# Optimization experiments

Measured on AMD Instinct MI355X. Metric: run time of the kernel, lower is better.

## Reference

```python
import jax, jax.numpy as jnp
import numpy as np

E = 300000        # num_edges
T = 3000000       # num_triplets
D = 128           # edge_message_dim
N_RAD = 6
N_SPH = 7
D_DOWN = 64       # edge_down_dim
D_BAS = 8         # basis_embed_dim


def _w(key, fan_in, fan_out):
    return jax.random.normal(key, (fan_in, fan_out), jnp.float32) / np.sqrt(fan_in)


def setup_inputs() -> dict:
    key = jax.random.key(0)
    ks = jax.random.split(key, 32)
    inp = {
        "x": jax.random.normal(ks[0], (E, D), jnp.float32),
        "rbf": jax.random.uniform(ks[1], (E, N_RAD), jnp.float32),
        "sbf": jax.random.uniform(ks[2], (T, N_SPH * N_RAD), jnp.float32),
        "idx_kj": jax.random.randint(ks[3], (T,), 0, E),
        "idx_ji": jax.random.randint(ks[4], (T,), 0, E),
        # basis projections (bias-free)
        "w_rbf1": _w(ks[5], N_RAD, D_BAS),
        "w_rbf2": _w(ks[6], D_BAS, D),
        "w_sbf1": _w(ks[7], N_SPH * N_RAD, D_BAS),
        "w_sbf2": _w(ks[8], D_BAS, D_DOWN),
        # message linears (with bias)
        "w_kj": _w(ks[9], D, D), "b_kj": jnp.zeros((D,), jnp.float32),
        "w_ji": _w(ks[10], D, D), "b_ji": jnp.zeros((D,), jnp.float32),
        # down / up projections (bias-free)
        "w_down": _w(ks[11], D, D_DOWN),
        "w_up": _w(ks[12], D_DOWN, D),
        # residual block before skip + dense
        "res1_w1": _w(ks[13], D, D), "res1_b1": jnp.zeros((D,), jnp.float32),
        "res1_w2": _w(ks[14], D, D), "res1_b2": jnp.zeros((D,), jnp.float32),
        "w_bs": _w(ks[15], D, D), "b_bs": jnp.zeros((D,), jnp.float32),
        # two residual blocks after skip
        "res2_w1": _w(ks[16], D, D), "res2_b1": jnp.zeros((D,), jnp.float32),
        "res2_w2": _w(ks[17], D, D), "res2_b2": jnp.zeros((D,), jnp.float32),
        "res3_w1": _w(ks[18], D, D), "res3_b1": jnp.zeros((D,), jnp.float32),
        "res3_w2": _w(ks[19], D, D), "res3_b2": jnp.zeros((D,), jnp.float32),
    }
    return inp


def _res_block(h, w1, b1, w2, b2):
    # h + act(lin2(act(lin1(h)))) with Swish(beta=1) == silu
    return h + jax.nn.silu(jax.nn.silu(h @ w1 + b1) @ w2 + b2)


def reference(x, rbf, sbf, idx_kj, idx_ji,
              w_rbf1, w_rbf2, w_sbf1, w_sbf2,
              w_kj, b_kj, w_ji, b_ji, w_down, w_up,
              res1_w1, res1_b1, res1_w2, res1_b2, w_bs, b_bs,
              res2_w1, res2_b1, res2_w2, res2_b2,
              res3_w1, res3_b1, res3_w2, res3_b2):
    act = jax.nn.silu
    x_ji = act(x @ w_ji + b_ji)                       # [E, D]
    x_kj = act(x @ w_kj + b_kj)                       # [E, D]
    rbf_e = (rbf @ w_rbf1) @ w_rbf2                   # [E, D]
    x_kj = act((x_kj * rbf_e) @ w_down)               # [E, D_DOWN]
    sbf_e = (sbf @ w_sbf1) @ w_sbf2                   # [T, D_DOWN]
    m = x_kj[idx_kj] * sbf_e                          # gather + Hadamard [T, D_DOWN]
    agg = jax.ops.segment_sum(m, idx_ji, num_segments=x.shape[0])  # [E, D_DOWN]
    x_kj = act(agg @ w_up)                            # [E, D]
    h = _res_block(x_ji + x_kj, res1_w1, res1_b1, res1_w2, res1_b2)
    h = act(h @ w_bs + b_bs) + x                      # skip connection
    h = _res_block(h, res2_w1, res2_b1, res2_w2, res2_b2)
    h = _res_block(h, res3_w1, res3_b1, res3_w2, res3_b2)
    return h
```

## Files before the change

kernel.cpp:

```cpp
#include <hip/hip_runtime.h>
#include <hip/hip_bf16.h>


typedef __attribute__((ext_vector_type(8))) short bf16x8;
typedef __attribute__((ext_vector_type(4))) float f32x4;
typedef __attribute__((ext_vector_type(4))) unsigned int u32x4;

__device__ __forceinline__ float silu_f(float v) {
    return v * __builtin_amdgcn_rcpf(1.0f + __expf(-v));
}
__device__ __forceinline__ short f2bf(float f) {
    unsigned u = __float_as_uint(f);
    unsigned r = u + 0x7fffu + ((u >> 16) & 1u);
    return (short)(r >> 16);
}
__device__ __forceinline__ float bf2f(short s) {
    return __uint_as_float(((unsigned)(unsigned short)s) << 16);
}

__device__ __forceinline__ unsigned cvt_pk_bf16(float a, float b) {
    __hip_bfloat162 h = __float22bfloat162_rn(float2{a, b});
    return *reinterpret_cast<unsigned*>(&h);
}
__device__ __forceinline__ void split44(f32x4 a, f32x4 b, bf16x8& hi, bf16x8& lo) {
    float f[8] = {a[0], a[1], a[2], a[3], b[0], b[1], b[2], b[3]};
    u32x4 H, L;
    #pragma unroll
    for (int j = 0; j < 4; ++j) {
        const float f0 = f[2 * j], f1 = f[2 * j + 1];
        const unsigned h = cvt_pk_bf16(f0, f1);
        const float r0 = f0 - __uint_as_float(h << 16);
        const float r1 = f1 - __uint_as_float(h & 0xffff0000u);
        H[j] = h;
        L[j] = cvt_pk_bf16(r0, r1);
    }
    hi = __builtin_bit_cast(bf16x8, H);
    lo = __builtin_bit_cast(bf16x8, L);
}

__device__ __forceinline__ void gll16(const void* g, void* l) {
    __builtin_amdgcn_global_load_lds((const __attribute__((address_space(1))) void*)g,
                                     (__attribute__((address_space(3))) void*)l, 16, 0, 0);
}
__device__ __forceinline__ void stage16(const char* g, short* l, int lane, int wid) {
    #pragma unroll
    for (int i = 0; i < 4; ++i) {
        const int off = ((i * 4 + wid) << 10);
        gll16(g + off + lane * 16, (char*)l + off);
    }
}
__device__ __forceinline__ void stage8(const char* g, short* l, int lane, int wid) {
    #pragma unroll
    for (int i = 0; i < 2; ++i) {
        const int off = ((i * 4 + wid) << 10);
        gll16(g + off + lane * 16, (char*)l + off);
    }
}

template<int NF>
__device__ __forceinline__ void mfma_ks(bf16x8 ah, bf16x8 al, const short* slot,
                                        int acol, int kq, f32x4* acc) {
    #pragma unroll
    for (int n = 0; n < NF; ++n) {
        const int c = n * 16 + acol;
        const int x = (c >> 2) & 1;
        const int sw = (kq ^ (c & 3)) << 3;
        const bf16x8 bh = *(const bf16x8*)&slot[c * 64 + x * 32 + sw];
        const bf16x8 bl = *(const bf16x8*)&slot[c * 64 + (x ^ 1) * 32 + sw];
        acc[n] = __builtin_amdgcn_mfma_f32_16x16x32_bf16(ah, bh, acc[n], 0, 0, 0);
        acc[n] = __builtin_amdgcn_mfma_f32_16x16x32_bf16(al, bh, acc[n], 0, 0, 0);
        acc[n] = __builtin_amdgcn_mfma_f32_16x16x32_bf16(ah, bl, acc[n], 0, 0, 0);
    }
}

__device__ __forceinline__ void tfrag(const float* tl, int rb, int q, int kq,
                                      bf16x8& Ah, bf16x8& Al) {
    const f32x4 ta = *(const f32x4*)&tl[rb + q * 32 + kq * 8];
    const f32x4 tb = *(const f32x4*)&tl[rb + q * 32 + kq * 8 + 4];
    split44(ta, tb, Ah, Al);
}

__device__ __forceinline__ void tgemm4(const char* img, const char* imgnext,
                                       short* sA, short* sB, const float* tl, int rb,
                                       int kq, int acol, int lane, int wid, f32x4* acc)
{
    bf16x8 Ah[4], Al[4];
    #pragma unroll
    for (int q = 0; q < 4; ++q) tfrag(tl, rb, q, kq, Ah[q], Al[q]);

    stage16(img + 16384, sB, lane, wid);
    mfma_ks<8>(Ah[0], Al[0], sA, acol, kq, acc); __syncthreads();
    stage16(img + 32768, sA, lane, wid);
    mfma_ks<8>(Ah[1], Al[1], sB, acol, kq, acc); __syncthreads();
    stage16(img + 49152, sB, lane, wid);
    mfma_ks<8>(Ah[2], Al[2], sA, acol, kq, acc); __syncthreads();
    if (imgnext) stage16(imgnext, sA, lane, wid);
    mfma_ks<8>(Ah[3], Al[3], sB, acol, kq, acc); __syncthreads();
}

#define TPITCH 132

struct WDesc { const float* src; char* dst; int K; int N; };
struct WPrepArgs { WDesc w[11]; };

__global__ void wprep_kernel(WPrepArgs args) {
    const WDesc d = args.w[blockIdx.y];
    const int h = blockIdx.x;
    if (h * 32 >= d.K) return;
    char* slab = d.dst + (size_t)h * d.N * 128;
    for (int idx = threadIdx.x; idx < d.N * 4; idx += 256) {
        const int c = idx >> 2, ch = idx & 3;
        bf16x8 hi, lo;
        #pragma unroll
        for (int j = 0; j < 8; ++j) {
            const float f = d.src[(size_t)(h * 32 + ch * 8 + j) * d.N + c];
            const short hb = f2bf(f);
            hi[j] = hb;
            lo[j] = f2bf(f - bf2f(hb));
        }
        const int x = (c >> 2) & 1;
        const int sw = (ch ^ (c & 3)) * 16;
        *(bf16x8*)(slab + c * 128 + x * 64 + sw)       = hi;
        *(bf16x8*)(slab + c * 128 + (x ^ 1) * 64 + sw) = lo;
    }
}


__global__ void rbf1_kernel(const float* __restrict__ rbf, const float* __restrict__ w_rbf1,
                            float* __restrict__ re1, int E) {
    const int i = blockIdx.x * 256 + threadIdx.x;
    const int e = i >> 3, p = i & 7;
    if (e < E) {
        float s = 0.f;
        #pragma unroll
        for (int q = 0; q < 6; ++q) s = fmaf(rbf[e * 6 + q], w_rbf1[q * 8 + p], s);
        re1[i] = s;
    }
}

__global__ void count_rank_kernel(const int* __restrict__ idx_ji, int* __restrict__ cnt,
                                  int* __restrict__ rank, int T) {
    const int i = (blockIdx.x * 256 + threadIdx.x) * 4;
    if (i + 3 < T) {
        const int4 j = *(const int4*)&idx_ji[i];
        int4 r;
        r.x = atomicAdd(&cnt[j.x], 1);
        r.y = atomicAdd(&cnt[j.y], 1);
        r.z = atomicAdd(&cnt[j.z], 1);
        r.w = atomicAdd(&cnt[j.w], 1);
        *(int4*)&rank[i] = r;
    } else {
        for (int k = i; k < T; ++k) rank[k] = atomicAdd(&cnt[idx_ji[k]], 1);
    }
}

__global__ void scan_partial_kernel(const int* __restrict__ cnt, int* __restrict__ partial, int E) {
    __shared__ int red[256];
    const int tid = threadIdx.x;
    const int base = blockIdx.x * 1024 + tid * 4;
    int s = 0;
    #pragma unroll
    for (int i = 0; i < 4; ++i) { const int g = base + i; if (g < E) s += cnt[g]; }
    red[tid] = s;
    __syncthreads();
    for (int off = 128; off > 0; off >>= 1) {
        if (tid < off) red[tid] += red[tid + off];
        __syncthreads();
    }
    if (tid == 0) partial[blockIdx.x] = red[0];
}

__global__ void scan_block_kernel(const int* __restrict__ partial, int* __restrict__ blockoff,
                                  int NB, int* offsets, int E) {
    __shared__ int red[256];
    const int tid = threadIdx.x;
    int v[4]; int s = 0;
    #pragma unroll
    for (int i = 0; i < 4; ++i) { const int g = tid * 4 + i; v[i] = (g < NB) ? partial[g] : 0; s += v[i]; }
    red[tid] = s;
    __syncthreads();
    for (int off = 1; off < 256; off <<= 1) {
        const int add = (tid >= off) ? red[tid - off] : 0;
        __syncthreads();
        red[tid] += add;
        __syncthreads();
    }
    int excl = (tid == 0) ? 0 : red[tid - 1];
    #pragma unroll
    for (int i = 0; i < 4; ++i) { const int g = tid * 4 + i; if (g < NB) blockoff[g] = excl; excl += v[i]; }
    if (tid == 255) offsets[E] = red[255];
}

__global__ void scan_final_kernel(const int* __restrict__ cnt, const int* __restrict__ blockoff,
                                  int* __restrict__ offsets, int E) {
    __shared__ int red[256];
    const int tid = threadIdx.x;
    const int base = blockIdx.x * 1024 + tid * 4;
    int v[4]; int s = 0;
    #pragma unroll
    for (int i = 0; i < 4; ++i) { const int g = base + i; v[i] = (g < E) ? cnt[g] : 0; s += v[i]; }
    red[tid] = s;
    __syncthreads();
    for (int off = 1; off < 256; off <<= 1) {
        const int add = (tid >= off) ? red[tid - off] : 0;
        __syncthreads();
        red[tid] += add;
        __syncthreads();
    }
    int run = blockoff[blockIdx.x] + ((tid == 0) ? 0 : red[tid - 1]);
    #pragma unroll
    for (int i = 0; i < 4; ++i) {
        const int g = base + i;
        if (g < E) offsets[g] = run;
        run += v[i];
    }
}

__launch_bounds__(256, 3)
__global__ void e1fill_kernel(const float* __restrict__ sbf, const float* __restrict__ w_sbf1,
                              const int* __restrict__ idx_ji, const int* __restrict__ idx_kj,
                              const int* __restrict__ rank, const int* __restrict__ offsets,
                              float* __restrict__ E1p, int* __restrict__ kjp, int T)
{
    __shared__ float s_lds[256 * 43];
    const int tid = threadIdx.x;
    const long long t0 = (long long)blockIdx.x * 256;
    const int nrow = min(256, (int)(T - t0));
    const int nel  = nrow * 42;
    const float* base = sbf + t0 * 42;

    for (int i = tid * 4; i + 3 < nel; i += 1024) {
        const float4 v = *(const float4*)&base[i];
        s_lds[(i + 0) + (i + 0) / 42] = v.x;
        s_lds[(i + 1) + (i + 1) / 42] = v.y;
        s_lds[(i + 2) + (i + 2) / 42] = v.z;
        s_lds[(i + 3) + (i + 3) / 42] = v.w;
    }
    const int tail0 = nel & ~3;
    if (tid < nel - tail0) { const int g = tail0 + tid; s_lds[g + g / 42] = base[g]; }
    __syncthreads();

    const int t = (int)t0 + tid;
    if (t >= T) return;
    const float* srow = &s_lds[tid * 43];
    float e1[8] = {0.f, 0.f, 0.f, 0.f, 0.f, 0.f, 0.f, 0.f};
    #pragma unroll
    for (int q = 0; q < 42; ++q) {
        const float s = srow[q];
        #pragma unroll
        for (int p = 0; p < 8; ++p) e1[p] = fmaf(s, w_sbf1[q * 8 + p], e1[p]);
    }
    const int ji  = idx_ji[t];
    const int pos = offsets[ji] + rank[t];
    *(float4*)&E1p[(size_t)pos * 8]     = *(float4*)&e1[0];
    *(float4*)&E1p[(size_t)pos * 8 + 4] = *(float4*)&e1[4];
    kjp[pos] = idx_kj[t];
}

__launch_bounds__(256, 4)
__global__ void gather_kernel(const float* __restrict__ E1p, const int* __restrict__ kjp,
                              const float* __restrict__ w_sbf2, const int* __restrict__ offsets,
                              const float* __restrict__ xkjd, float* __restrict__ agg, int E)
{
    const int tid  = threadIdx.x;
    const int lane = tid & 63;
    const int e    = blockIdx.x * 4 + (tid >> 6);

    float w2[8];
    #pragma unroll
    for (int p = 0; p < 8; ++p) w2[p] = w_sbf2[p * 64 + lane];

    if (e >= E) return;
    const int j0 = __builtin_amdgcn_readfirstlane(offsets[e]);
    const int j1 = __builtin_amdgcn_readfirstlane(offsets[e + 1]);

    float acc = 0.f;
    if (j0 < j1) {
        int kj = __builtin_amdgcn_readfirstlane(kjp[j0]);
        float4 ea = *(const float4*)&E1p[(size_t)j0 * 8];
        float4 eb = *(const float4*)&E1p[(size_t)j0 * 8 + 4];
        float xv = xkjd[(size_t)kj * 64 + lane];
        for (int j = j0; j < j1; ++j) {
            float xn = 0.f; float4 ean = {}, ebn = {};
            if (j + 1 < j1) {
                const int kn = __builtin_amdgcn_readfirstlane(kjp[j + 1]);
                ean = *(const float4*)&E1p[(size_t)(j + 1) * 8];
                ebn = *(const float4*)&E1p[(size_t)(j + 1) * 8 + 4];
                xn  = xkjd[(size_t)kn * 64 + lane];
            }
            float sv = ea.x * w2[0];
            sv = fmaf(ea.y, w2[1], sv);
            sv = fmaf(ea.z, w2[2], sv);
            sv = fmaf(ea.w, w2[3], sv);
            sv = fmaf(eb.x, w2[4], sv);
            sv = fmaf(eb.y, w2[5], sv);
            sv = fmaf(eb.z, w2[6], sv);
            sv = fmaf(eb.w, w2[7], sv);
            acc = fmaf(xv, sv, acc);
            ea = ean; eb = ebn; xv = xn;
        }
    }
    agg[(size_t)e * 64 + lane] = acc;
}

__launch_bounds__(256, 2)
__global__ void k1_kernel(const float* __restrict__ x, const char* __restrict__ wkj_i,
                          const float* __restrict__ b_kj, const float* __restrict__ re1,
                          const float* __restrict__ w_rbf2, const char* __restrict__ wdn_i,
                          float* __restrict__ W3, int E)
{
    __shared__ short slotA[8192], slotB[8192];
    __shared__ float t_lds[64 * TPITCH];
    __shared__ float w2_lds[8 * 128];
    const int tid = threadIdx.x, lane = tid & 63, wid = tid >> 6;
    const int acol = lane & 15, kq = lane >> 4;
    const int rowW = blockIdx.x * 64 + wid * 16;
    const int arow = rowW + acol;
    const bool av = arow < E;

    stage16(wkj_i, slotA, lane, wid);
    const float* xr = x + (size_t)arow * 128;
    bf16x8 aH[4], aL[4];
    #pragma unroll
    for (int ks = 0; ks < 4; ++ks) {
        f32x4 a0 = f32x4{0.f, 0.f, 0.f, 0.f}, a1 = f32x4{0.f, 0.f, 0.f, 0.f};
        if (av) { a0 = *(const f32x4*)&xr[ks * 32 + kq * 8];
                  a1 = *(const f32x4*)&xr[ks * 32 + kq * 8 + 4]; }
        split44(a0, a1, aH[ks], aL[ks]);
    }
    float bv[8];
    #pragma unroll
    for (int n = 0; n < 8; ++n) bv[n] = b_kj[n * 16 + acol];
    f32x4 e1a[4], e1b[4];
    #pragma unroll
    for (int r = 0; r < 4; ++r) {
        const int ge = rowW + kq * 4 + r;
        e1a[r] = f32x4{0.f, 0.f, 0.f, 0.f}; e1b[r] = f32x4{0.f, 0.f, 0.f, 0.f};
        if (ge < E) { e1a[r] = *(const f32x4*)&re1[(size_t)ge * 8];
                      e1b[r] = *(const f32x4*)&re1[(size_t)ge * 8 + 4]; }
    }
    for (int i = tid; i < 1024; i += 256) w2_lds[i] = w_rbf2[i];
    __syncthreads();

    f32x4 acc[8];
    #pragma unroll
    for (int n = 0; n < 8; ++n) acc[n] = f32x4{0.f, 0.f, 0.f, 0.f};

    stage16(wkj_i + 16384, slotB, lane, wid);
    mfma_ks<8>(aH[0], aL[0], slotA, acol, kq, acc); __syncthreads();
    stage16(wkj_i + 32768, slotA, lane, wid);
    mfma_ks<8>(aH[1], aL[1], slotB, acol, kq, acc); __syncthreads();
    stage16(wkj_i + 49152, slotB, lane, wid);
    mfma_ks<8>(aH[2], aL[2], slotA, acol, kq, acc); __syncthreads();
    stage8(wdn_i, slotA, lane, wid);
    mfma_ks<8>(aH[3], aL[3], slotB, acol, kq, acc); __syncthreads();

    #pragma unroll
    for (int n = 0; n < 8; ++n) {
        const int c = n * 16 + acol;
        float w2c[8];
        #pragma unroll
        for (int p = 0; p < 8; ++p) w2c[p] = w2_lds[p * 128 + c];
        #pragma unroll
        for (int r = 0; r < 4; ++r) {
            float s = e1a[r][0] * w2c[0];
            s = fmaf(e1a[r][1], w2c[1], s);
            s = fmaf(e1a[r][2], w2c[2], s);
            s = fmaf(e1a[r][3], w2c[3], s);
            s = fmaf(e1b[r][0], w2c[4], s);
            s = fmaf(e1b[r][1], w2c[5], s);
            s = fmaf(e1b[r][2], w2c[6], s);
            s = fmaf(e1b[r][3], w2c[7], s);
            t_lds[(wid * 16 + kq * 4 + r) * TPITCH + c] = silu_f(acc[n][r] + bv[n]) * s;
        }
    }
    __syncthreads();

    f32x4 acc2[4];
    #pragma unroll
    for (int n = 0; n < 4; ++n) acc2[n] = f32x4{0.f, 0.f, 0.f, 0.f};
    const int rb = (wid * 16 + acol) * TPITCH;

    bf16x8 tH[4], tL[4];
    #pragma unroll
    for (int q = 0; q < 4; ++q) tfrag(t_lds, rb, q, kq, tH[q], tL[q]);

    stage8(wdn_i + 8192, slotB, lane, wid);
    mfma_ks<4>(tH[0], tL[0], slotA, acol, kq, acc2); __syncthreads();
    stage8(wdn_i + 16384, slotA, lane, wid);
    mfma_ks<4>(tH[1], tL[1], slotB, acol, kq, acc2); __syncthreads();
    stage8(wdn_i + 24576, slotB, lane, wid);
    mfma_ks<4>(tH[2], tL[2], slotA, acol, kq, acc2); __syncthreads();
    mfma_ks<4>(tH[3], tL[3], slotB, acol, kq, acc2);

    #pragma unroll
    for (int n = 0; n < 4; ++n) {
        const int c = n * 16 + acol;
        #pragma unroll
        for (int r = 0; r < 4; ++r) {
            const int ge = rowW + kq * 4 + r;
            if (ge < E) W3[(size_t)ge * 64 + c] = silu_f(acc2[n][r]);
        }
    }
}

struct KBigArgs {
    const float* x; const float* W4; float* out;
    const char *wji, *wup, *r1w1, *r1w2, *wbs, *r2w1, *r2w2, *r3w1, *r3w2;
    const float *bji, *r1b1, *r1b2, *bbs, *r2b1, *r2b2, *r3b1, *r3b2;
    int E;
};

__launch_bounds__(256, 2)
__global__ void kbig_kernel(KBigArgs A_)
{
    __shared__ short slotA[8192], slotB[8192];
    __shared__ float t_lds[64 * TPITCH];
    const int tid = threadIdx.x, lane = tid & 63, wid = tid >> 6;
    const int acol = lane & 15, kq = lane >> 4;
    const int rowW = blockIdx.x * 64 + wid * 16;
    const int arow = rowW + acol;
    const int E = A_.E;
    const bool av = arow < E;
    const int rb = (wid * 16 + acol) * TPITCH;

    stage16(A_.wji, slotA, lane, wid);

    const float* xr = A_.x + (size_t)arow * 128;
    const float* wr = A_.W4 + (size_t)arow * 64;
    bf16x8 aH[4], aL[4], uH[2], uL[2];
    #pragma unroll
    for (int ks = 0; ks < 4; ++ks) {
        f32x4 a0 = f32x4{0.f, 0.f, 0.f, 0.f}, a1 = f32x4{0.f, 0.f, 0.f, 0.f};
        if (av) { a0 = *(const f32x4*)&xr[ks * 32 + kq * 8];
                  a1 = *(const f32x4*)&xr[ks * 32 + kq * 8 + 4]; }
        split44(a0, a1, aH[ks], aL[ks]);
    }
    #pragma unroll
    for (int ks = 0; ks < 2; ++ks) {
        f32x4 u0 = f32x4{0.f, 0.f, 0.f, 0.f}, u1 = f32x4{0.f, 0.f, 0.f, 0.f};
        if (av) { u0 = *(const f32x4*)&wr[ks * 32 + kq * 8];
                  u1 = *(const f32x4*)&wr[ks * 32 + kq * 8 + 4]; }
        split44(u0, u1, uH[ks], uL[ks]);
    }
    __syncthreads();

    f32x4 acc[8];
    #pragma unroll
    for (int n = 0; n < 8; ++n) acc[n] = f32x4{0.f, 0.f, 0.f, 0.f};

    stage16(A_.wji + 16384, slotB, lane, wid);
    mfma_ks<8>(aH[0], aL[0], slotA, acol, kq, acc); __syncthreads();
    stage16(A_.wji + 32768, slotA, lane, wid);
    mfma_ks<8>(aH[1], aL[1], slotB, acol, kq, acc); __syncthreads();
    stage16(A_.wji + 49152, slotB, lane, wid);
    mfma_ks<8>(aH[2], aL[2], slotA, acol, kq, acc); __syncthreads();
    stage16(A_.wup, slotA, lane, wid);
    mfma_ks<8>(aH[3], aL[3], slotB, acol, kq, acc); __syncthreads();

    float res[8][4];
    #pragma unroll
    for (int n = 0; n < 8; ++n) {
        const float bv = A_.bji[n * 16 + acol];
        #pragma unroll
        for (int r = 0; r < 4; ++r) { res[n][r] = silu_f(acc[n][r] + bv); acc[n][r] = 0.f; }
    }

    stage16(A_.wup + 16384, slotB, lane, wid);
    mfma_ks<8>(uH[0], uL[0], slotA, acol, kq, acc); __syncthreads();
    stage16(A_.r1w1, slotA, lane, wid);
    mfma_ks<8>(uH[1], uL[1], slotB, acol, kq, acc); __syncthreads();

    #pragma unroll
    for (int n = 0; n < 8; ++n) {
        const int c = n * 16 + acol;
        #pragma unroll
        for (int r = 0; r < 4; ++r) {
            res[n][r] += silu_f(acc[n][r]);
            t_lds[(wid * 16 + kq * 4 + r) * TPITCH + c] = res[n][r];
            acc[n][r] = 0.f;
        }
    }
    __syncthreads();

    tgemm4(A_.r1w1, A_.r1w2, slotA, slotB, t_lds, rb, kq, acol, lane, wid, acc);
    #pragma unroll
    for (int n = 0; n < 8; ++n) {
        const float bv = A_.r1b1[n * 16 + acol];
        const int c = n * 16 + acol;
        #pragma unroll
        for (int r = 0; r < 4; ++r) {
            t_lds[(wid * 16 + kq * 4 + r) * TPITCH + c] = silu_f(acc[n][r] + bv);
            acc[n][r] = 0.f;
        }
    }
    __syncthreads();

    tgemm4(A_.r1w2, A_.wbs, slotA, slotB, t_lds, rb, kq, acol, lane, wid, acc);
    #pragma unroll
    for (int n = 0; n < 8; ++n) {
        const float bv = A_.r1b2[n * 16 + acol];
        const int c = n * 16 + acol;
        #pragma unroll
        for (int r = 0; r < 4; ++r) {
            t_lds[(wid * 16 + kq * 4 + r) * TPITCH + c] = res[n][r] + silu_f(acc[n][r] + bv);
            acc[n][r] = 0.f;
        }
    }
    __syncthreads();

    tgemm4(A_.wbs, A_.r2w1, slotA, slotB, t_lds, rb, kq, acol, lane, wid, acc);
    #pragma unroll
    for (int n = 0; n < 8; ++n) {
        const float bv = A_.bbs[n * 16 + acol];
        const int c = n * 16 + acol;
        #pragma unroll
        for (int r = 0; r < 4; ++r) {
            const int ge = rowW + kq * 4 + r;
            const float xv = (ge < E) ? A_.x[(size_t)ge * 128 + c] : 0.f;
            res[n][r] = silu_f(acc[n][r] + bv) + xv;
            t_lds[(wid * 16 + kq * 4 + r) * TPITCH + c] = res[n][r];
            acc[n][r] = 0.f;
        }
    }
    __syncthreads();

    tgemm4(A_.r2w1, A_.r2w2, slotA, slotB, t_lds, rb, kq, acol, lane, wid, acc);
    #pragma unroll
    for (int n = 0; n < 8; ++n) {
        const float bv = A_.r2b1[n * 16 + acol];
        const int c = n * 16 + acol;
        #pragma unroll
        for (int r = 0; r < 4; ++r) {
            t_lds[(wid * 16 + kq * 4 + r) * TPITCH + c] = silu_f(acc[n][r] + bv);
            acc[n][r] = 0.f;
        }
    }
    __syncthreads();

    tgemm4(A_.r2w2, A_.r3w1, slotA, slotB, t_lds, rb, kq, acol, lane, wid, acc);
    #pragma unroll
    for (int n = 0; n < 8; ++n) {
        const float bv = A_.r2b2[n * 16 + acol];
        const int c = n * 16 + acol;
        #pragma unroll
        for (int r = 0; r < 4; ++r) {
            res[n][r] += silu_f(acc[n][r] + bv);
            t_lds[(wid * 16 + kq * 4 + r) * TPITCH + c] = res[n][r];
            acc[n][r] = 0.f;
        }
    }
    __syncthreads();

    tgemm4(A_.r3w1, A_.r3w2, slotA, slotB, t_lds, rb, kq, acol, lane, wid, acc);
    #pragma unroll
    for (int n = 0; n < 8; ++n) {
        const float bv = A_.r3b1[n * 16 + acol];
        const int c = n * 16 + acol;
        #pragma unroll
        for (int r = 0; r < 4; ++r) {
            t_lds[(wid * 16 + kq * 4 + r) * TPITCH + c] = silu_f(acc[n][r] + bv);
            acc[n][r] = 0.f;
        }
    }
    __syncthreads();

    tgemm4(A_.r3w2, nullptr, slotA, slotB, t_lds, rb, kq, acol, lane, wid, acc);
    #pragma unroll
    for (int n = 0; n < 8; ++n) {
        const float bv = A_.r3b2[n * 16 + acol];
        const int c = n * 16 + acol;
        #pragma unroll
        for (int r = 0; r < 4; ++r) {
            const int ge = rowW + kq * 4 + r;
            if (ge < E)
                A_.out[(size_t)ge * 128 + c] = res[n][r] + silu_f(acc[n][r] + bv);
        }
    }
}


extern "C" void kernel_launch(void* const* d_in, const int* in_sizes, int n_in,
                              void* d_out, int out_size, void* d_ws, size_t ws_size,
                              hipStream_t stream)
{
    const float* x      = (const float*)d_in[0];
    const float* rbf    = (const float*)d_in[1];
    const float* sbf    = (const float*)d_in[2];
    const int*   idx_kj = (const int*)d_in[3];
    const int*   idx_ji = (const int*)d_in[4];
    const float* w_rbf1 = (const float*)d_in[5];
    const float* w_rbf2 = (const float*)d_in[6];
    const float* w_sbf1 = (const float*)d_in[7];
    const float* w_sbf2 = (const float*)d_in[8];
    const float* w_kj   = (const float*)d_in[9];
    const float* b_kj   = (const float*)d_in[10];
    const float* w_ji   = (const float*)d_in[11];
    const float* b_ji   = (const float*)d_in[12];
    const float* w_down = (const float*)d_in[13];
    const float* w_up   = (const float*)d_in[14];
    const float* r1w1   = (const float*)d_in[15];
    const float* r1b1   = (const float*)d_in[16];
    const float* r1w2   = (const float*)d_in[17];
    const float* r1b2   = (const float*)d_in[18];
    const float* w_bs   = (const float*)d_in[19];
    const float* b_bs   = (const float*)d_in[20];
    const float* r2w1   = (const float*)d_in[21];
    const float* r2b1   = (const float*)d_in[22];
    const float* r2w2   = (const float*)d_in[23];
    const float* r2b2   = (const float*)d_in[24];
    const float* r3w1   = (const float*)d_in[25];
    const float* r3b1   = (const float*)d_in[26];
    const float* r3w2   = (const float*)d_in[27];
    const float* r3b2   = (const float*)d_in[28];

    const int E = in_sizes[0] / 128;
    const int T = in_sizes[2] / 42;

    float* OUT = (float*)d_out;
    float* W3  = (float*)((char*)d_ws + (size_t)E * 128 * 4);
    float* W4  = (float*)((char*)d_ws + (size_t)E * 128 * 4
                                      + (size_t)E * 64 * 4);

    int*   cnt      = (int*)d_ws;
    int*   offsets  = cnt + (E + 64);
    int*   partial  = offsets + (E + 64);
    int*   blockoff = partial + 1024;
    float* E1p      = (float*)((char*)d_ws + (4u << 20));
    int*   kjp      = (int*)((char*)d_ws + (102u << 20));
    float* re1      = (float*)((char*)d_ws + (116u << 20));
    char*  wimg     = (char*)d_ws + (130u << 20);
    int*   rank     = (int*)((char*)d_ws + (134u << 20));

    char* wkj_i  = wimg;
    char* wji_i  = wimg + 65536;
    char* wdn_i  = wimg + 131072;
    char* wup_i  = wimg + 163840;
    char* r1w1_i = wimg + 196608;
    char* r1w2_i = wimg + 262144;
    char* wbs_i  = wimg + 327680;
    char* r2w1_i = wimg + 393216;
    char* r2w2_i = wimg + 458752;
    char* r3w1_i = wimg + 524288;
    char* r3w2_i = wimg + 589824;

    WPrepArgs pa;
    pa.w[0]  = {w_kj,   wkj_i,  128, 128};
    pa.w[1]  = {w_ji,   wji_i,  128, 128};
    pa.w[2]  = {w_down, wdn_i,  128,  64};
    pa.w[3]  = {w_up,   wup_i,   64, 128};
    pa.w[4]  = {r1w1,   r1w1_i, 128, 128};
    pa.w[5]  = {r1w2,   r1w2_i, 128, 128};
    pa.w[6]  = {w_bs,   wbs_i,  128, 128};
    pa.w[7]  = {r2w1,   r2w1_i, 128, 128};
    pa.w[8]  = {r2w2,   r2w2_i, 128, 128};
    pa.w[9]  = {r3w1,   r3w1_i, 128, 128};
    pa.w[10] = {r3w2,   r3w2_i, 128, 128};

    const dim3 b256(256);
    const int gB  = (E + 63) / 64;
    const int gT  = (T + 255) / 256;
    const int gT4 = (T + 1023) / 1024;
    const int NB  = (E + 1023) / 1024;
    const int gE4 = (E + 3) / 4;
    const int gR  = (E * 8 + 255) / 256;

    wprep_kernel<<<dim3(4, 11), b256, 0, stream>>>(pa);
    rbf1_kernel<<<gR, b256, 0, stream>>>(rbf, w_rbf1, re1, E);
    hipMemsetAsync(cnt, 0, (size_t)E * 4, stream);
    count_rank_kernel<<<gT4, b256, 0, stream>>>(idx_ji, cnt, rank, T);
    scan_partial_kernel<<<NB, b256, 0, stream>>>(cnt, partial, E);
    scan_block_kernel<<<1, b256, 0, stream>>>(partial, blockoff, NB, offsets, E);
    scan_final_kernel<<<NB, b256, 0, stream>>>(cnt, blockoff, offsets, E);
    e1fill_kernel<<<gT, b256, 0, stream>>>(sbf, w_sbf1, idx_ji, idx_kj, rank, offsets, E1p, kjp, T);

    k1_kernel<<<gB, b256, 0, stream>>>(x, wkj_i, b_kj, re1, w_rbf2, wdn_i, W3, E);
    gather_kernel<<<gE4, b256, 0, stream>>>(E1p, kjp, w_sbf2, offsets, W3, W4, E);

    KBigArgs ka;
    ka.x = x; ka.W4 = W4; ka.out = OUT;
    ka.wji = wji_i; ka.wup = wup_i; ka.r1w1 = r1w1_i; ka.r1w2 = r1w2_i; ka.wbs = wbs_i;
    ka.r2w1 = r2w1_i; ka.r2w2 = r2w2_i; ka.r3w1 = r3w1_i; ka.r3w2 = r3w2_i;
    ka.bji = b_ji; ka.r1b1 = r1b1; ka.r1b2 = r1b2; ka.bbs = b_bs;
    ka.r2b1 = r2b1; ka.r2b2 = r2b2; ka.r3b1 = r3b1; ka.r3b2 = r3b2;
    ka.E = E;
    kbig_kernel<<<gB, b256, 0, stream>>>(ka);
}
```

Baseline: 1.201 ms.

## Switch dense GEMMs from 3-pass bf16 split to 2-pass fp16 split

Replaces the bf16 hi/lo split (three MFMAs per tile: hi*hi, lo*hi, hi*lo) with an fp16 scheme: activations are split into fp16 hi/lo, weights are stored as a single fp16 copy, and two MFMAs run per tile. This halves the weight image size and the LDS staging buffers, and drops a third of the MFMA work. The smaller LDS footprint allows raising launch bounds to 3 blocks per CU for higher occupancy. The risk is reduced accuracy: weights carry only fp16 precision, and fp16's narrower exponent range could overflow or underflow on large or tiny activations.

```diff
diff --git a/kernel.cpp b/kernel.cpp
--- a/kernel.cpp
+++ b/kernel.cpp
@@ -2,99 +2,74 @@
 #include <hip/hip_bf16.h>
 
 
-typedef __attribute__((ext_vector_type(8))) short bf16x8;
+typedef __attribute__((ext_vector_type(8))) _Float16 f16x8;
 typedef __attribute__((ext_vector_type(4))) float f32x4;
-typedef __attribute__((ext_vector_type(4))) unsigned int u32x4;
 
 __device__ __forceinline__ float silu_f(float v) {
     return v * __builtin_amdgcn_rcpf(1.0f + __expf(-v));
 }
-__device__ __forceinline__ short f2bf(float f) {
-    unsigned u = __float_as_uint(f);
-    unsigned r = u + 0x7fffu + ((u >> 16) & 1u);
-    return (short)(r >> 16);
-}
-__device__ __forceinline__ float bf2f(short s) {
-    return __uint_as_float(((unsigned)(unsigned short)s) << 16);
-}
-
-__device__ __forceinline__ unsigned cvt_pk_bf16(float a, float b) {
-    __hip_bfloat162 h = __float22bfloat162_rn(float2{a, b});
-    return *reinterpret_cast<unsigned*>(&h);
-}
-__device__ __forceinline__ void split44(f32x4 a, f32x4 b, bf16x8& hi, bf16x8& lo) {
+
+__device__ __forceinline__ void split44h(f32x4 a, f32x4 b, f16x8& hi, f16x8& lo) {
     float f[8] = {a[0], a[1], a[2], a[3], b[0], b[1], b[2], b[3]};
-    u32x4 H, L;
-    #pragma unroll
-    for (int j = 0; j < 4; ++j) {
-        const float f0 = f[2 * j], f1 = f[2 * j + 1];
-        const unsigned h = cvt_pk_bf16(f0, f1);
-        const float r0 = f0 - __uint_as_float(h << 16);
-        const float r1 = f1 - __uint_as_float(h & 0xffff0000u);
-        H[j] = h;
-        L[j] = cvt_pk_bf16(r0, r1);
-    }
-    hi = __builtin_bit_cast(bf16x8, H);
-    lo = __builtin_bit_cast(bf16x8, L);
+    #pragma unroll
+    for (int j = 0; j < 8; ++j) {
+        const _Float16 h = (_Float16)f[j];
+        hi[j] = h;
+        lo[j] = (_Float16)(f[j] - (float)h);
+    }
 }
 
 __device__ __forceinline__ void gll16(const void* g, void* l) {
     __builtin_amdgcn_global_load_lds((const __attribute__((address_space(1))) void*)g,
                                      (__attribute__((address_space(3))) void*)l, 16, 0, 0);
 }
-__device__ __forceinline__ void stage16(const char* g, short* l, int lane, int wid) {
-    #pragma unroll
-    for (int i = 0; i < 4; ++i) {
-        const int off = ((i * 4 + wid) << 10);
-        gll16(g + off + lane * 16, (char*)l + off);
-    }
-}
-__device__ __forceinline__ void stage8(const char* g, short* l, int lane, int wid) {
+__device__ __forceinline__ void stage8k(const char* g, _Float16* l, int lane, int wid) {
     #pragma unroll
     for (int i = 0; i < 2; ++i) {
         const int off = ((i * 4 + wid) << 10);
         gll16(g + off + lane * 16, (char*)l + off);
     }
 }
+__device__ __forceinline__ void stage4k(const char* g, _Float16* l, int lane, int wid) {
+    const int off = (wid << 10);
+    gll16(g + off + lane * 16, (char*)l + off);
+}
 
 template<int NF>
-__device__ __forceinline__ void mfma_ks(bf16x8 ah, bf16x8 al, const short* slot,
+__device__ __forceinline__ void mfma_ks(f16x8 ah, f16x8 al, const _Float16* slot,
                                         int acol, int kq, f32x4* acc) {
     #pragma unroll
     for (int n = 0; n < NF; ++n) {
         const int c = n * 16 + acol;
-        const int x = (c >> 2) & 1;
         const int sw = (kq ^ (c & 3)) << 3;
-        const bf16x8 bh = *(const bf16x8*)&slot[c * 64 + x * 32 + sw];
-        const bf16x8 bl = *(const bf16x8*)&slot[c * 64 + (x ^ 1) * 32 + sw];
-        acc[n] = __builtin_amdgcn_mfma_f32_16x16x32_bf16(ah, bh, acc[n], 0, 0, 0);
-        acc[n] = __builtin_amdgcn_mfma_f32_16x16x32_bf16(al, bh, acc[n], 0, 0, 0);
-        acc[n] = __builtin_amdgcn_mfma_f32_16x16x32_bf16(ah, bl, acc[n], 0, 0, 0);
+        const f16x8 bh = *(const f16x8*)&slot[c * 32 + sw];
+        acc[n] = __builtin_amdgcn_mfma_f32_16x16x32_f16(ah, bh, acc[n], 0, 0, 0);
+        acc[n] = __builtin_amdgcn_mfma_f32_16x16x32_f16(al, bh, acc[n], 0, 0, 0);
     }
 }
 
 __device__ __forceinline__ void tfrag(const float* tl, int rb, int q, int kq,
-                                      bf16x8& Ah, bf16x8& Al) {
+                                      f16x8& Ah, f16x8& Al) {
     const f32x4 ta = *(const f32x4*)&tl[rb + q * 32 + kq * 8];
     const f32x4 tb = *(const f32x4*)&tl[rb + q * 32 + kq * 8 + 4];
-    split44(ta, tb, Ah, Al);
+    split44h(ta, tb, Ah, Al);
 }
 
 __device__ __forceinline__ void tgemm4(const char* img, const char* imgnext,
-                                       short* sA, short* sB, const float* tl, int rb,
+                                       _Float16* sA, _Float16* sB, const float* tl, int rb,
                                        int kq, int acol, int lane, int wid, f32x4* acc)
 {
-    bf16x8 Ah[4], Al[4];
+    f16x8 Ah[4], Al[4];
     #pragma unroll
     for (int q = 0; q < 4; ++q) tfrag(tl, rb, q, kq, Ah[q], Al[q]);
 
-    stage16(img + 16384, sB, lane, wid);
+    stage8k(img + 8192, sB, lane, wid);
     mfma_ks<8>(Ah[0], Al[0], sA, acol, kq, acc); __syncthreads();
-    stage16(img + 32768, sA, lane, wid);
+    stage8k(img + 16384, sA, lane, wid);
     mfma_ks<8>(Ah[1], Al[1], sB, acol, kq, acc); __syncthreads();
-    stage16(img + 49152, sB, lane, wid);
+    stage8k(img + 24576, sB, lane, wid);
     mfma_ks<8>(Ah[2], Al[2], sA, acol, kq, acc); __syncthreads();
-    if (imgnext) stage16(imgnext, sA, lane, wid);
+    if (imgnext) stage8k(imgnext, sA, lane, wid);
     mfma_ks<8>(Ah[3], Al[3], sB, acol, kq, acc); __syncthreads();
 }
 
@@ -107,21 +82,14 @@
     const WDesc d = args.w[blockIdx.y];
     const int h = blockIdx.x;
     if (h * 32 >= d.K) return;
-    char* slab = d.dst + (size_t)h * d.N * 128;
+    char* slab = d.dst + (size_t)h * d.N * 64;
     for (int idx = threadIdx.x; idx < d.N * 4; idx += 256) {
         const int c = idx >> 2, ch = idx & 3;
-        bf16x8 hi, lo;
-        #pragma unroll
-        for (int j = 0; j < 8; ++j) {
-            const float f = d.src[(size_t)(h * 32 + ch * 8 + j) * d.N + c];
-            const short hb = f2bf(f);
-            hi[j] = hb;
-            lo[j] = f2bf(f - bf2f(hb));
-        }
-        const int x = (c >> 2) & 1;
-        const int sw = (ch ^ (c & 3)) * 16;
-        *(bf16x8*)(slab + c * 128 + x * 64 + sw)       = hi;
-        *(bf16x8*)(slab + c * 128 + (x ^ 1) * 64 + sw) = lo;
+        f16x8 v;
+        #pragma unroll
+        for (int j = 0; j < 8; ++j)
+            v[j] = (_Float16)d.src[(size_t)(h * 32 + ch * 8 + j) * d.N + c];
+        *(f16x8*)(slab + c * 64 + ((ch ^ (c & 3)) << 4)) = v;
     }
 }
 
@@ -303,13 +271,13 @@
     agg[(size_t)e * 64 + lane] = acc;
 }
 
-__launch_bounds__(256, 2)
+__launch_bounds__(256, 3)
 __global__ void k1_kernel(const float* __restrict__ x, const char* __restrict__ wkj_i,
                           const float* __restrict__ b_kj, const float* __restrict__ re1,
                           const float* __restrict__ w_rbf2, const char* __restrict__ wdn_i,
                           float* __restrict__ W3, int E)
 {
-    __shared__ short slotA[8192], slotB[8192];
+    __shared__ _Float16 slotA[4096], slotB[4096];
     __shared__ float t_lds[64 * TPITCH];
     __shared__ float w2_lds[8 * 128];
     const int tid = threadIdx.x, lane = tid & 63, wid = tid >> 6;
@@ -318,15 +286,15 @@
     const int arow = rowW + acol;
     const bool av = arow < E;
 
-    stage16(wkj_i, slotA, lane, wid);
+    stage8k(wkj_i, slotA, lane, wid);
     const float* xr = x + (size_t)arow * 128;
-    bf16x8 aH[4], aL[4];
+    f16x8 aH[4], aL[4];
     #pragma unroll
     for (int ks = 0; ks < 4; ++ks) {
         f32x4 a0 = f32x4{0.f, 0.f, 0.f, 0.f}, a1 = f32x4{0.f, 0.f, 0.f, 0.f};
         if (av) { a0 = *(const f32x4*)&xr[ks * 32 + kq * 8];
                   a1 = *(const f32x4*)&xr[ks * 32 + kq * 8 + 4]; }
-        split44(a0, a1, aH[ks], aL[ks]);
+        split44h(a0, a1, aH[ks], aL[ks]);
     }
     float bv[8];
     #pragma unroll
@@ -346,13 +314,13 @@
     #pragma unroll
     for (int n = 0; n < 8; ++n) acc[n] = f32x4{0.f, 0.f, 0.f, 0.f};
 
-    stage16(wkj_i + 16384, slotB, lane, wid);
+    stage8k(wkj_i + 8192, slotB, lane, wid);
     mfma_ks<8>(aH[0], aL[0], slotA, acol, kq, acc); __syncthreads();
-    stage16(wkj_i + 32768, slotA, lane, wid);
+    stage8k(wkj_i + 16384, slotA, lane, wid);
     mfma_ks<8>(aH[1], aL[1], slotB, acol, kq, acc); __syncthreads();
-    stage16(wkj_i + 49152, slotB, lane, wid);
+    stage8k(wkj_i + 24576, slotB, lane, wid);
     mfma_ks<8>(aH[2], aL[2], slotA, acol, kq, acc); __syncthreads();
-    stage8(wdn_i, slotA, lane, wid);
+    stage4k(wdn_i, slotA, lane, wid);
     mfma_ks<8>(aH[3], aL[3], slotB, acol, kq, acc); __syncthreads();
 
     #pragma unroll
@@ -381,15 +349,15 @@
     for (int n = 0; n < 4; ++n) acc2[n] = f32x4{0.f, 0.f, 0.f, 0.f};
     const int rb = (wid * 16 + acol) * TPITCH;
 
-    bf16x8 tH[4], tL[4];
+    f16x8 tH[4], tL[4];
     #pragma unroll
     for (int q = 0; q < 4; ++q) tfrag(t_lds, rb, q, kq, tH[q], tL[q]);
 
-    stage8(wdn_i + 8192, slotB, lane, wid);
+    stage4k(wdn_i + 4096, slotB, lane, wid);
     mfma_ks<4>(tH[0], tL[0], slotA, acol, kq, acc2); __syncthreads();
-    stage8(wdn_i + 16384, slotA, lane, wid);
+    stage4k(wdn_i + 8192, slotA, lane, wid);
     mfma_ks<4>(tH[1], tL[1], slotB, acol, kq, acc2); __syncthreads();
-    stage8(wdn_i + 24576, slotB, lane, wid);
+    stage4k(wdn_i + 12288, slotB, lane, wid);
     mfma_ks<4>(tH[2], tL[2], slotA, acol, kq, acc2); __syncthreads();
     mfma_ks<4>(tH[3], tL[3], slotB, acol, kq, acc2);
 
@@ -411,10 +379,10 @@
     int E;
 };
 
-__launch_bounds__(256, 2)
+__launch_bounds__(256, 3)
 __global__ void kbig_kernel(KBigArgs A_)
 {
-    __shared__ short slotA[8192], slotB[8192];
+    __shared__ _Float16 slotA[4096], slotB[4096];
     __shared__ float t_lds[64 * TPITCH];
     const int tid = threadIdx.x, lane = tid & 63, wid = tid >> 6;
     const int acol = lane & 15, kq = lane >> 4;
@@ -424,24 +392,24 @@
     const bool av = arow < E;
     const int rb = (wid * 16 + acol) * TPITCH;
 
-    stage16(A_.wji, slotA, lane, wid);
+    stage8k(A_.wji, slotA, lane, wid);
 
     const float* xr = A_.x + (size_t)arow * 128;
     const float* wr = A_.W4 + (size_t)arow * 64;
-    bf16x8 aH[4], aL[4], uH[2], uL[2];
+    f16x8 aH[4], aL[4], uH[2], uL[2];
     #pragma unroll
     for (int ks = 0; ks < 4; ++ks) {
         f32x4 a0 = f32x4{0.f, 0.f, 0.f, 0.f}, a1 = f32x4{0.f, 0.f, 0.f, 0.f};
         if (av) { a0 = *(const f32x4*)&xr[ks * 32 + kq * 8];
                   a1 = *(const f32x4*)&xr[ks * 32 + kq * 8 + 4]; }
-        split44(a0, a1, aH[ks], aL[ks]);
+        split44h(a0, a1, aH[ks], aL[ks]);
     }
     #pragma unroll
     for (int ks = 0; ks < 2; ++ks) {
         f32x4 u0 = f32x4{0.f, 0.f, 0.f, 0.f}, u1 = f32x4{0.f, 0.f, 0.f, 0.f};
         if (av) { u0 = *(const f32x4*)&wr[ks * 32 + kq * 8];
                   u1 = *(const f32x4*)&wr[ks * 32 + kq * 8 + 4]; }
-        split44(u0, u1, uH[ks], uL[ks]);
+        split44h(u0, u1, uH[ks], uL[ks]);
     }
     __syncthreads();
 
@@ -449,13 +417,13 @@
     #pragma unroll
     for (int n = 0; n < 8; ++n) acc[n] = f32x4{0.f, 0.f, 0.f, 0.f};
 
-    stage16(A_.wji + 16384, slotB, lane, wid);
+    stage8k(A_.wji + 8192, slotB, lane, wid);
     mfma_ks<8>(aH[0], aL[0], slotA, acol, kq, acc); __syncthreads();
-    stage16(A_.wji + 32768, slotA, lane, wid);
+    stage8k(A_.wji + 16384, slotA, lane, wid);
     mfma_ks<8>(aH[1], aL[1], slotB, acol, kq, acc); __syncthreads();
-    stage16(A_.wji + 49152, slotB, lane, wid);
+    stage8k(A_.wji + 24576, slotB, lane, wid);
     mfma_ks<8>(aH[2], aL[2], slotA, acol, kq, acc); __syncthreads();
-    stage16(A_.wup, slotA, lane, wid);
+    stage8k(A_.wup, slotA, lane, wid);
     mfma_ks<8>(aH[3], aL[3], slotB, acol, kq, acc); __syncthreads();
 
     float res[8][4];
@@ -466,9 +434,9 @@
         for (int r = 0; r < 4; ++r) { res[n][r] = silu_f(acc[n][r] + bv); acc[n][r] = 0.f; }
     }
 
-    stage16(A_.wup + 16384, slotB, lane, wid);
+    stage8k(A_.wup + 8192, slotB, lane, wid);
     mfma_ks<8>(uH[0], uL[0], slotA, acol, kq, acc); __syncthreads();
-    stage16(A_.r1w1, slotA, lane, wid);
+    stage8k(A_.r1w1, slotA, lane, wid);
     mfma_ks<8>(uH[1], uL[1], slotB, acol, kq, acc); __syncthreads();
 
     #pragma unroll
@@ -633,16 +601,16 @@
     int*   rank     = (int*)((char*)d_ws + (134u << 20));
 
     char* wkj_i  = wimg;
-    char* wji_i  = wimg + 65536;
-    char* wdn_i  = wimg + 131072;
-    char* wup_i  = wimg + 163840;
-    char* r1w1_i = wimg + 196608;
-    char* r1w2_i = wimg + 262144;
-    char* wbs_i  = wimg + 327680;
-    char* r2w1_i = wimg + 393216;
-    char* r2w2_i = wimg + 458752;
-    char* r3w1_i = wimg + 524288;
-    char* r3w2_i = wimg + 589824;
+    char* wji_i  = wimg + 32768;
+    char* wdn_i  = wimg + 65536;
+    char* wup_i  = wimg + 81920;
+    char* r1w1_i = wimg + 98304;
+    char* r1w2_i = wimg + 131072;
+    char* wbs_i  = wimg + 163840;
+    char* r2w1_i = wimg + 196608;
+    char* r2w2_i = wimg + 229376;
+    char* r3w1_i = wimg + 262144;
+    char* r3w2_i = wimg + 294912;
 
     WPrepArgs pa;
     pa.w[0]  = {w_kj,   wkj_i,  128, 128};
```

New measurement: 1.020 ms. 1.18x faster.
